# Performance work log

Measured on AMD Instinct MI355X. Metric: run time of the kernel, lower is better.

Reference implementation:

```python
import jax, jax.numpy as jnp
import numpy as np

N_NODES = 100000
N_EDGES = 1600000
D_IN = 128
D_OUT = 128


def setup_inputs() -> dict:
    key = jax.random.key(0)
    k1, k2, k3, k4, k5, k6 = jax.random.split(key, 6)
    x = jax.random.normal(k1, (N_NODES, D_IN), dtype=jnp.float32)
    edge_src = jax.random.randint(k2, (N_EDGES,), 0, N_NODES, dtype=jnp.int64 if jax.config.jax_enable_x64 else jnp.int32)
    edge_dst = jax.random.randint(k3, (N_EDGES,), 0, N_NODES, dtype=jnp.int64 if jax.config.jax_enable_x64 else jnp.int32)
    edge_val = jax.random.uniform(k4, (N_EDGES,), dtype=jnp.float32)
    # nn.Linear(2*D_IN, D_OUT): store W as [2*D_IN, D_OUT] (transposed torch layout)
    W = jax.random.normal(k5, (2 * D_IN, D_OUT), dtype=jnp.float32) * (1.0 / np.sqrt(2 * D_IN))
    b = jax.random.normal(k6, (D_OUT,), dtype=jnp.float32) * 0.01
    return {"x": x, "edge_src": edge_src, "edge_dst": edge_dst, "edge_val": edge_val, "W": W, "b": b}


def reference(x, edge_src, edge_dst, edge_val, W, b):
    # support = adj @ x  (sparse COO: adj[dst, src] = edge_val)
    gathered = x[edge_src] * edge_val[:, None]               # [E, D_IN]
    support = jax.ops.segment_sum(gathered, edge_dst, num_segments=x.shape[0])  # [N, D_IN]
    # concat self + aggregated neighbor features, then linear
    h = jnp.concatenate([x, support], axis=1)                # [N, 2*D_IN]
    return h @ W + b                                          # [N, D_OUT]
```

## Files before the change

### kernel.cpp

```cpp
#include <hip/hip_runtime.h>

#define D 128
#define NBMAX 2048
#define CHUNK 2048
#define BN 64
#define GCAP 2048

typedef __attribute__((ext_vector_type(8))) short bf16x8;
typedef __attribute__((ext_vector_type(4))) float f32x4;

__device__ __forceinline__ unsigned short f2bf(float f) {
    unsigned int u = __builtin_bit_cast(unsigned int, f);
    u = (u + 0x7fffu + ((u >> 16) & 1u)) >> 16;
    return (unsigned short)u;
}
__device__ __forceinline__ float bf2f(unsigned int u) {
    return __builtin_bit_cast(float, u << 16);
}

__global__ void zero_int_kernel(int* __restrict__ p, int n) {
    int i = blockIdx.x * 256 + threadIdx.x;
    if (i < n) p[i] = 0;
}

__global__ void xprep_kernel(const float* __restrict__ x,
                             unsigned short* __restrict__ x_bf, int n4) {
    int i = blockIdx.x * 256 + threadIdx.x;
    if (i >= n4) return;
    float4 v = ((const float4*)x)[i];
    ushort4 s; s.x = f2bf(v.x); s.y = f2bf(v.y); s.z = f2bf(v.z); s.w = f2bf(v.w);
    ((ushort4*)x_bf)[i] = s;
}

__global__ void wprep_kernel(const float* __restrict__ W,
                             unsigned short* __restrict__ WT) {
    int t = blockIdx.x * 256 + threadIdx.x;
    int col = t & 127, k = t >> 7;
    WT[col * 256 + k] = f2bf(W[k * D + col]);
}

__global__ __launch_bounds__(256) void bhist_kernel(const int* __restrict__ edst,
                                                    int* __restrict__ bucket_cnt,
                                                    int E, int NB) {
    __shared__ int h[NBMAX];
    for (int i = threadIdx.x; i < NB; i += 256) h[i] = 0;
    __syncthreads();
    int stride = gridDim.x * 256;
    for (int e = blockIdx.x * 256 + threadIdx.x; e < E; e += stride)
        atomicAdd(&h[edst[e] >> 6], 1);
    __syncthreads();
    for (int i = threadIdx.x; i < NB; i += 256) {
        int c = h[i];
        if (c) atomicAdd(&bucket_cnt[i], c);
    }
}

__global__ __launch_bounds__(256) void bscan_kernel(const int* __restrict__ cnt,
                                                    int* __restrict__ base,
                                                    int* __restrict__ cursor, int NB) {
    __shared__ int p[256];
    int t = threadIdx.x;
    int c[8]; int loc = 0;
#pragma unroll
    for (int k = 0; k < 8; ++k) {
        int i = t * 8 + k;
        c[k] = (i < NB) ? cnt[i] : 0;
        loc += c[k];
    }
    p[t] = loc;
    __syncthreads();
    for (int off = 1; off < 256; off <<= 1) {
        int v = p[t];
        int u = (t >= off) ? p[t - off] : 0;
        __syncthreads();
        p[t] = v + u;
        __syncthreads();
    }
    int ex = p[t] - loc;
#pragma unroll
    for (int k = 0; k < 8; ++k) {
        int i = t * 8 + k;
        if (i < NB) { base[i] = ex; cursor[i] = ex; }
        ex += c[k];
    }
}

__global__ __launch_bounds__(256) void bfill_kernel(const int* __restrict__ esrc,
                                                    const int* __restrict__ edst,
                                                    const float* __restrict__ eval,
                                                    int* __restrict__ bucket_cursor,
                                                    int2* __restrict__ edge_pack,
                                                    int E, int NB) {
    __shared__ int lh[NBMAX];
    __shared__ int lcur[NBMAX];
    __shared__ int p[256];
    __shared__ int2 ord[CHUNK];
    __shared__ unsigned short obk[CHUNK];

    const int tid = threadIdx.x;
    const int base = blockIdx.x * CHUNK;
    const int n = min(CHUNK, E - base);

    for (int i = tid; i < NBMAX; i += 256) lh[i] = 0;
    __syncthreads();

    int esv[8]; int ebk[8];
    float evv[8];
#pragma unroll
    for (int k = 0; k < 8; ++k) {
        int li = k * 256 + tid;
        if (li < n) {
            int i = base + li;
            int dst = edst[i];
            esv[k] = esrc[i];
            evv[k] = eval[i];
            int b = dst >> 6;
            ebk[k] = b | ((dst & 63) << 16);
            atomicAdd(&lh[b], 1);
        } else ebk[k] = -1;
    }
    __syncthreads();

    int s[8]; int loc = 0;
#pragma unroll
    for (int k = 0; k < 8; ++k) { s[k] = lh[8 * tid + k]; loc += s[k]; }
    p[tid] = loc;
    __syncthreads();
    for (int off = 1; off < 256; off <<= 1) {
        int v = p[tid];
        int u = (tid >= off) ? p[tid - off] : 0;
        __syncthreads();
        p[tid] = v + u;
        __syncthreads();
    }
    int ex = p[tid] - loc;
#pragma unroll
    for (int k = 0; k < 8; ++k) { lcur[8 * tid + k] = ex; ex += s[k]; }
    __syncthreads();

#pragma unroll
    for (int k = 0; k < 8; ++k) {
        if (ebk[k] >= 0) {
            int b = ebk[k] & 0xffff, nl = ebk[k] >> 16;
            int slot = atomicAdd(&lcur[b], 1);
            ord[slot] = make_int2(esv[k] | (nl << 20), __builtin_bit_cast(int, evv[k]));
            obk[slot] = (unsigned short)b;
        }
    }
    __syncthreads();

    for (int b = tid; b < NB; b += 256) {
        int c = lh[b];
        if (c) lh[b] = atomicAdd(&bucket_cursor[b], c) - (lcur[b] - c);
    }
    __syncthreads();

    for (int i = tid; i < n; i += 256) {
        int b = obk[i];
        edge_pack[lh[b] + i] = ord[i];
    }
}

__global__ __launch_bounds__(256, 4) void gather_fused_kernel(
        const unsigned short* __restrict__ x_bf,
        const int* __restrict__ bucket_base,
        const int* __restrict__ bucket_cnt,
        const int2* __restrict__ edge_pack,
        const unsigned short* __restrict__ WT,
        const float* __restrict__ bias,
        float* __restrict__ out, int N) {
    __shared__ unsigned short accb[BN * 136];
    __shared__ int2 ord[GCAP];
    __shared__ int cnt64[BN];
    __shared__ int start64[BN + 1];
    __shared__ int cur64[BN];

    const int tid = threadIdx.x;
    const int b = blockIdx.x;
    const int start = bucket_base[b];
    const int cnt = bucket_cnt[b];
    const int node0 = b * BN;
    const int w = tid >> 6, lane = tid & 63;
    unsigned int* accw = (unsigned int*)accb;

    for (int i = tid * 8; i < BN * 136; i += 2048)
        *(uint4*)(accb + i) = make_uint4(0u, 0u, 0u, 0u);

    for (int c0 = 0; c0 < cnt; c0 += GCAP) {
        const int n = min(GCAP, cnt - c0);
        if (tid < BN) cnt64[tid] = 0;
        __syncthreads();
        for (int i = tid; i < n; i += 256)
            atomicAdd(&cnt64[(edge_pack[start + c0 + i].x >> 20) & 63], 1);
        __syncthreads();
        if (tid < BN) {
            int c = cnt64[tid];
            int v = c;
#pragma unroll
            for (int off = 1; off < 64; off <<= 1) {
                int t = __shfl_up(v, off, 64);
                if (lane >= off) v += t;
            }
            start64[tid] = v - c;
            cur64[tid] = v - c;
            if (tid == BN - 1) start64[BN] = v;
        }
        __syncthreads();
        for (int i = tid; i < n; i += 256) {
            int2 e = edge_pack[start + c0 + i];
            ord[atomicAdd(&cur64[(e.x >> 20) & 63], 1)] = e;
        }
        __syncthreads();

        const int js = start64[w * 16];
        const int je = start64[w * 16 + 16];
        int cur = -1;
        float ax = 0.f, ay = 0.f;
        for (int g = js; g < je; g += 16) {
            int m = je - g; if (m > 16) m = 16;
            int2 e[16];
#pragma unroll
            for (int k = 0; k < 16; ++k) {
                int idx = g + k; if (idx >= je) idx = je - 1;
                e[k] = ord[idx];
            }
            unsigned int p[16];
#pragma unroll
            for (int k = 0; k < 16; ++k)
                p[k] = *(const unsigned int*)(x_bf + (size_t)(e[k].x & 0xFFFFF) * D + lane * 2);
#pragma unroll
            for (int k = 0; k < 16; ++k) {
                if (k < m) {
                    int nd = (e[k].x >> 20) & 63;
                    if (nd != cur) {
                        if (cur >= 0) {
                            unsigned int o = accw[cur * 68 + lane];
                            float o0 = bf2f(o & 0xffffu) + ax;
                            float o1 = bf2f(o >> 16) + ay;
                            accw[cur * 68 + lane] =
                                (unsigned int)f2bf(o0) | ((unsigned int)f2bf(o1) << 16);
                        }
                        cur = nd; ax = 0.f; ay = 0.f;
                    }
                    float v = __builtin_bit_cast(float, e[k].y);
                    ax += bf2f(p[k] & 0xffffu) * v;
                    ay += bf2f(p[k] >> 16) * v;
                }
            }
        }
        if (cur >= 0) {
            unsigned int o = accw[cur * 68 + lane];
            float o0 = bf2f(o & 0xffffu) + ax;
            float o1 = bf2f(o >> 16) + ay;
            accw[cur * 68 + lane] = (unsigned int)f2bf(o0) | ((unsigned int)f2bf(o1) << 16);
        }
        __syncthreads();
    }

    const int quad = lane >> 4;
    const int l15  = lane & 15;
    const int colbase = w * 32;

    f32x4 acc[4][2];
#pragma unroll
    for (int rt = 0; rt < 4; ++rt) {
        acc[rt][0] = (f32x4){0.f, 0.f, 0.f, 0.f};
        acc[rt][1] = (f32x4){0.f, 0.f, 0.f, 0.f};
    }

#pragma unroll
    for (int ks = 0; ks < 8; ++ks) {
        bf16x8 wf0 = *(const bf16x8*)(WT + (size_t)(colbase + l15) * 256 + ks * 32 + quad * 8);
        bf16x8 wf1 = *(const bf16x8*)(WT + (size_t)(colbase + 16 + l15) * 256 + ks * 32 + quad * 8);
#pragma unroll
        for (int rt = 0; rt < 4; ++rt) {
            int row = rt * 16 + l15;
            bf16x8 a;
            if (ks < 4) {
                int rg = node0 + row; if (rg >= N) rg = N - 1;
                a = *(const bf16x8*)(x_bf + (size_t)rg * D + ks * 32 + quad * 8);
            } else {
                a = *(const bf16x8*)(accb + row * 136 + (ks - 4) * 32 + quad * 8);
            }
            acc[rt][0] = __builtin_amdgcn_mfma_f32_16x16x32_bf16(a, wf0, acc[rt][0], 0, 0, 0);
            acc[rt][1] = __builtin_amdgcn_mfma_f32_16x16x32_bf16(a, wf1, acc[rt][1], 0, 0, 0);
        }
    }

#pragma unroll
    for (int ct = 0; ct < 2; ++ct) {
        int col = colbase + ct * 16 + l15;
        float bv = bias[col];
#pragma unroll
        for (int rt = 0; rt < 4; ++rt) {
#pragma unroll
            for (int rg = 0; rg < 4; ++rg) {
                int row = node0 + rt * 16 + quad * 4 + rg;
                if (row < N)
                    out[(size_t)row * D + col] = acc[rt][ct][rg] + bv;
            }
        }
    }
}

extern "C" void kernel_launch(void* const* d_in, const int* in_sizes, int n_in,
                              void* d_out, int out_size, void* d_ws, size_t ws_size,
                              hipStream_t stream) {
    const float* x    = (const float*)d_in[0];
    const int*   esrc = (const int*)d_in[1];
    const int*   edst = (const int*)d_in[2];
    const float* eval = (const float*)d_in[3];
    const float* W    = (const float*)d_in[4];
    const float* bias = (const float*)d_in[5];
    float*       out  = (float*)d_out;

    const int N = in_sizes[0] / D;
    const int E = in_sizes[1];
    const int NB = (N + BN - 1) / BN;

    char* ws = (char*)d_ws;
    unsigned short* x_bf       = (unsigned short*)ws;
    int2*           edge_pack  = (int2*)(ws + 25600000);
    unsigned short* WT         = (unsigned short*)(ws + 38400000);
    int*            bucket_cnt = (int*)(ws + 38465536);
    int*            bucket_base= (int*)(ws + 38473728);
    int*            bucket_cur = (int*)(ws + 38481920);

    zero_int_kernel<<<(NB + 255) / 256, 256, 0, stream>>>(bucket_cnt, NB);
    xprep_kernel<<<(N * D / 4 + 255) / 256, 256, 0, stream>>>(x, x_bf, N * D / 4);
    wprep_kernel<<<(2 * D * D) / 256, 256, 0, stream>>>(W, WT);
    bhist_kernel<<<512, 256, 0, stream>>>(edst, bucket_cnt, E, NB);
    bscan_kernel<<<1, 256, 0, stream>>>(bucket_cnt, bucket_base, bucket_cur, NB);
    bfill_kernel<<<(E + CHUNK - 1) / CHUNK, 256, 0, stream>>>(esrc, edst, eval,
                                                              bucket_cur, edge_pack, E, NB);
    gather_fused_kernel<<<NB, 256, 0, stream>>>(x_bf, bucket_base, bucket_cnt,
                                                edge_pack, WT, bias, out, N);
}
```

Before: 274.8 us.

## Replace bucket sort with per-node counting sort and simplify gather

```diff
diff --git a/kernel.cpp b/kernel.cpp
--- a/kernel.cpp
+++ b/kernel.cpp
@@ -1,10 +1,7 @@
 #include <hip/hip_runtime.h>
 
 #define D 128
-#define NBMAX 2048
-#define CHUNK 2048
 #define BN 64
-#define GCAP 2048
 
 typedef __attribute__((ext_vector_type(8))) short bf16x8;
 typedef __attribute__((ext_vector_type(4))) float f32x4;
@@ -18,55 +15,93 @@
     return __builtin_bit_cast(float, u << 16);
 }
 
-__global__ void zero_int_kernel(int* __restrict__ p, int n) {
-    int i = blockIdx.x * 256 + threadIdx.x;
-    if (i < n) p[i] = 0;
-}
-
-__global__ void xprep_kernel(const float* __restrict__ x,
-                             unsigned short* __restrict__ x_bf, int n4) {
-    int i = blockIdx.x * 256 + threadIdx.x;
-    if (i >= n4) return;
-    float4 v = ((const float4*)x)[i];
-    ushort4 s; s.x = f2bf(v.x); s.y = f2bf(v.y); s.z = f2bf(v.z); s.w = f2bf(v.w);
-    ((ushort4*)x_bf)[i] = s;
-}
-
-__global__ void wprep_kernel(const float* __restrict__ W,
-                             unsigned short* __restrict__ WT) {
-    int t = blockIdx.x * 256 + threadIdx.x;
-    int col = t & 127, k = t >> 7;
-    WT[col * 256 + k] = f2bf(W[k * D + col]);
-}
-
-__global__ __launch_bounds__(256) void bhist_kernel(const int* __restrict__ edst,
-                                                    int* __restrict__ bucket_cnt,
-                                                    int E, int NB) {
-    __shared__ int h[NBMAX];
-    for (int i = threadIdx.x; i < NB; i += 256) h[i] = 0;
-    __syncthreads();
+__global__ void prep_kernel(const float* __restrict__ x,
+                            unsigned short* __restrict__ x_bf,
+                            const float* __restrict__ W,
+                            unsigned short* __restrict__ WT,
+                            int* __restrict__ nc,
+                            int n4, int XB, int WB, int NN) {
+    int blk = blockIdx.x, tid = threadIdx.x;
+    if (blk < XB) {
+        int i = blk * 256 + tid;
+        if (i < n4) {
+            float4 v = ((const float4*)x)[i];
+            ushort4 s;
+            s.x = f2bf(v.x); s.y = f2bf(v.y); s.z = f2bf(v.z); s.w = f2bf(v.w);
+            ((ushort4*)x_bf)[i] = s;
+        }
+    } else if (blk < XB + WB) {
+        int t = (blk - XB) * 256 + tid;
+        if (t < 2 * D * D) {
+            int col = t & 127, k = t >> 7;
+            WT[col * 256 + k] = f2bf(W[k * D + col]);
+        }
+    } else {
+        int i = (blk - XB - WB) * 256 + tid;
+        if (i < NN) nc[i] = 0;
+    }
+}
+
+__global__ void nhist_kernel(const int* __restrict__ edst,
+                             int* __restrict__ nc, int E) {
     int stride = gridDim.x * 256;
-    for (int e = blockIdx.x * 256 + threadIdx.x; e < E; e += stride)
-        atomicAdd(&h[edst[e] >> 6], 1);
-    __syncthreads();
-    for (int i = threadIdx.x; i < NB; i += 256) {
-        int c = h[i];
-        if (c) atomicAdd(&bucket_cnt[i], c);
-    }
-}
-
-__global__ __launch_bounds__(256) void bscan_kernel(const int* __restrict__ cnt,
-                                                    int* __restrict__ base,
-                                                    int* __restrict__ cursor, int NB) {
+    for (int i = blockIdx.x * 256 + threadIdx.x; i < E; i += stride)
+        atomicAdd(&nc[edst[i]], 1);
+}
+
+__global__ __launch_bounds__(256) void scanA_kernel(const int* __restrict__ nc,
+                                                    int* __restrict__ psum, int NN) {
     __shared__ int p[256];
     int t = threadIdx.x;
-    int c[8]; int loc = 0;
-#pragma unroll
-    for (int k = 0; k < 8; ++k) {
-        int i = t * 8 + k;
-        c[k] = (i < NB) ? cnt[i] : 0;
-        loc += c[k];
-    }
+    int i0 = blockIdx.x * 1024 + t * 4;
+    int s = 0;
+    if (i0 + 3 < NN) {
+        int4 v = *(const int4*)(nc + i0);
+        s = v.x + v.y + v.z + v.w;
+    } else {
+#pragma unroll
+        for (int k = 0; k < 4; ++k) { int i = i0 + k; if (i < NN) s += nc[i]; }
+    }
+    p[t] = s;
+    __syncthreads();
+    for (int off = 128; off > 0; off >>= 1) {
+        if (t < off) p[t] += p[t + off];
+        __syncthreads();
+    }
+    if (t == 0) psum[blockIdx.x] = p[0];
+}
+
+__global__ void scanB_kernel(const int* __restrict__ psum,
+                             int* __restrict__ pbase, int nparts) {
+    __shared__ int q[128];
+    int t = threadIdx.x;
+    int s = (t < nparts) ? psum[t] : 0;
+    q[t] = s;
+    __syncthreads();
+    for (int off = 1; off < 128; off <<= 1) {
+        int v = q[t];
+        int u = (t >= off) ? q[t - off] : 0;
+        __syncthreads();
+        q[t] = v + u;
+        __syncthreads();
+    }
+    if (t < nparts) pbase[t] = q[t] - s;
+}
+
+__global__ __launch_bounds__(256) void scanC_kernel(int* __restrict__ nc,
+                                                    const int* __restrict__ pbase, int NN) {
+    __shared__ int p[256];
+    int t = threadIdx.x, blk = blockIdx.x;
+    int i0 = blk * 1024 + t * 4;
+    int c[4];
+    if (i0 + 3 < NN) {
+        int4 v = *(const int4*)(nc + i0);
+        c[0] = v.x; c[1] = v.y; c[2] = v.z; c[3] = v.w;
+    } else {
+#pragma unroll
+        for (int k = 0; k < 4; ++k) { int i = i0 + k; c[k] = (i < NN) ? nc[i] : 0; }
+    }
+    int loc = c[0] + c[1] + c[2] + c[3];
     p[t] = loc;
     __syncthreads();
     for (int off = 1; off < 256; off <<= 1) {
@@ -76,186 +111,88 @@
         p[t] = v + u;
         __syncthreads();
     }
-    int ex = p[t] - loc;
-#pragma unroll
-    for (int k = 0; k < 8; ++k) {
-        int i = t * 8 + k;
-        if (i < NB) { base[i] = ex; cursor[i] = ex; }
-        ex += c[k];
-    }
-}
-
-__global__ __launch_bounds__(256) void bfill_kernel(const int* __restrict__ esrc,
-                                                    const int* __restrict__ edst,
-                                                    const float* __restrict__ eval,
-                                                    int* __restrict__ bucket_cursor,
-                                                    int2* __restrict__ edge_pack,
-                                                    int E, int NB) {
-    __shared__ int lh[NBMAX];
-    __shared__ int lcur[NBMAX];
-    __shared__ int p[256];
-    __shared__ int2 ord[CHUNK];
-    __shared__ unsigned short obk[CHUNK];
-
-    const int tid = threadIdx.x;
-    const int base = blockIdx.x * CHUNK;
-    const int n = min(CHUNK, E - base);
-
-    for (int i = tid; i < NBMAX; i += 256) lh[i] = 0;
-    __syncthreads();
-
-    int esv[8]; int ebk[8];
-    float evv[8];
-#pragma unroll
-    for (int k = 0; k < 8; ++k) {
-        int li = k * 256 + tid;
-        if (li < n) {
-            int i = base + li;
-            int dst = edst[i];
-            esv[k] = esrc[i];
-            evv[k] = eval[i];
-            int b = dst >> 6;
-            ebk[k] = b | ((dst & 63) << 16);
-            atomicAdd(&lh[b], 1);
-        } else ebk[k] = -1;
-    }
-    __syncthreads();
-
-    int s[8]; int loc = 0;
-#pragma unroll
-    for (int k = 0; k < 8; ++k) { s[k] = lh[8 * tid + k]; loc += s[k]; }
-    p[tid] = loc;
-    __syncthreads();
-    for (int off = 1; off < 256; off <<= 1) {
-        int v = p[tid];
-        int u = (tid >= off) ? p[tid - off] : 0;
-        __syncthreads();
-        p[tid] = v + u;
-        __syncthreads();
-    }
-    int ex = p[tid] - loc;
-#pragma unroll
-    for (int k = 0; k < 8; ++k) { lcur[8 * tid + k] = ex; ex += s[k]; }
-    __syncthreads();
-
-#pragma unroll
-    for (int k = 0; k < 8; ++k) {
-        if (ebk[k] >= 0) {
-            int b = ebk[k] & 0xffff, nl = ebk[k] >> 16;
-            int slot = atomicAdd(&lcur[b], 1);
-            ord[slot] = make_int2(esv[k] | (nl << 20), __builtin_bit_cast(int, evv[k]));
-            obk[slot] = (unsigned short)b;
-        }
-    }
-    __syncthreads();
-
-    for (int b = tid; b < NB; b += 256) {
-        int c = lh[b];
-        if (c) lh[b] = atomicAdd(&bucket_cursor[b], c) - (lcur[b] - c);
-    }
-    __syncthreads();
-
-    for (int i = tid; i < n; i += 256) {
-        int b = obk[i];
-        edge_pack[lh[b] + i] = ord[i];
-    }
-}
-
-__global__ __launch_bounds__(256, 4) void gather_fused_kernel(
+    int ex = p[t] - loc + pbase[blk];
+    int4 o;
+    ex += c[0]; o.x = ex;
+    ex += c[1]; o.y = ex;
+    ex += c[2]; o.z = ex;
+    ex += c[3]; o.w = ex;
+    *(int4*)(nc + i0) = o;
+}
+
+__global__ void nscatter_kernel(const int* __restrict__ esrc,
+                                const int* __restrict__ edst,
+                                const float* __restrict__ eval,
+                                int* __restrict__ nc,
+                                int2* __restrict__ edge_pack, int E) {
+    int stride = gridDim.x * 256;
+    for (int i = blockIdx.x * 256 + threadIdx.x; i < E; i += stride) {
+        int dst = edst[i];
+        int src = esrc[i];
+        float v = eval[i];
+        int pos = atomicSub(&nc[dst], 1) - 1;
+        edge_pack[pos] = make_int2((src << 8) | (dst & 63), __builtin_bit_cast(int, v));
+    }
+}
+
+__global__ __launch_bounds__(256, 8) void gather_fused_kernel(
         const unsigned short* __restrict__ x_bf,
-        const int* __restrict__ bucket_base,
-        const int* __restrict__ bucket_cnt,
+        const int* __restrict__ node_start,
         const int2* __restrict__ edge_pack,
         const unsigned short* __restrict__ WT,
         const float* __restrict__ bias,
         float* __restrict__ out, int N) {
     __shared__ unsigned short accb[BN * 136];
-    __shared__ int2 ord[GCAP];
-    __shared__ int cnt64[BN];
-    __shared__ int start64[BN + 1];
-    __shared__ int cur64[BN];
+    __shared__ int nb[BN + 1];
 
     const int tid = threadIdx.x;
     const int b = blockIdx.x;
-    const int start = bucket_base[b];
-    const int cnt = bucket_cnt[b];
     const int node0 = b * BN;
     const int w = tid >> 6, lane = tid & 63;
     unsigned int* accw = (unsigned int*)accb;
 
     for (int i = tid * 8; i < BN * 136; i += 2048)
         *(uint4*)(accb + i) = make_uint4(0u, 0u, 0u, 0u);
-
-    for (int c0 = 0; c0 < cnt; c0 += GCAP) {
-        const int n = min(GCAP, cnt - c0);
-        if (tid < BN) cnt64[tid] = 0;
-        __syncthreads();
-        for (int i = tid; i < n; i += 256)
-            atomicAdd(&cnt64[(edge_pack[start + c0 + i].x >> 20) & 63], 1);
-        __syncthreads();
-        if (tid < BN) {
-            int c = cnt64[tid];
-            int v = c;
-#pragma unroll
-            for (int off = 1; off < 64; off <<= 1) {
-                int t = __shfl_up(v, off, 64);
-                if (lane >= off) v += t;
+    if (tid <= BN) nb[tid] = node_start[node0 + tid];
+    __syncthreads();
+
+    const int js = __builtin_amdgcn_readfirstlane(nb[w * 16]);
+    const int je = __builtin_amdgcn_readfirstlane(nb[w * 16 + 16]);
+    const unsigned short* xl = x_bf + lane * 2;
+
+    int cur = -1;
+    float ax = 0.f, ay = 0.f;
+    for (int g = js; g < je; g += 16) {
+        int m = je - g; if (m > 16) m = 16;
+        int2 e[16];
+#pragma unroll
+        for (int k = 0; k < 16; ++k) {
+            int idx = g + k; if (idx >= je) idx = je - 1;
+            e[k] = edge_pack[idx];
+        }
+        unsigned int p[16];
+#pragma unroll
+        for (int k = 0; k < 16; ++k)
+            p[k] = *(const unsigned int*)(xl + ((e[k].x >> 8) << 7));
+#pragma unroll
+        for (int k = 0; k < 16; ++k) {
+            if (k < m) {
+                int nd = e[k].x & 63;
+                if (nd != cur) {
+                    if (cur >= 0)
+                        accw[cur * 68 + lane] =
+                            (unsigned int)f2bf(ax) | ((unsigned int)f2bf(ay) << 16);
+                    cur = nd; ax = 0.f; ay = 0.f;
+                }
+                float v = __builtin_bit_cast(float, e[k].y);
+                ax += bf2f(p[k] & 0xffffu) * v;
+                ay += bf2f(p[k] >> 16) * v;
             }
-            start64[tid] = v - c;
-            cur64[tid] = v - c;
-            if (tid == BN - 1) start64[BN] = v;
-        }
-        __syncthreads();
-        for (int i = tid; i < n; i += 256) {
-            int2 e = edge_pack[start + c0 + i];
-            ord[atomicAdd(&cur64[(e.x >> 20) & 63], 1)] = e;
-        }
-        __syncthreads();
-
-        const int js = start64[w * 16];
-        const int je = start64[w * 16 + 16];
-        int cur = -1;
-        float ax = 0.f, ay = 0.f;
-        for (int g = js; g < je; g += 16) {
-            int m = je - g; if (m > 16) m = 16;
-            int2 e[16];
-#pragma unroll
-            for (int k = 0; k < 16; ++k) {
-                int idx = g + k; if (idx >= je) idx = je - 1;
-                e[k] = ord[idx];
-            }
-            unsigned int p[16];
-#pragma unroll
-            for (int k = 0; k < 16; ++k)
-                p[k] = *(const unsigned int*)(x_bf + (size_t)(e[k].x & 0xFFFFF) * D + lane * 2);
-#pragma unroll
-            for (int k = 0; k < 16; ++k) {
-                if (k < m) {
-                    int nd = (e[k].x >> 20) & 63;
-                    if (nd != cur) {
-                        if (cur >= 0) {
-                            unsigned int o = accw[cur * 68 + lane];
-                            float o0 = bf2f(o & 0xffffu) + ax;
-                            float o1 = bf2f(o >> 16) + ay;
-                            accw[cur * 68 + lane] =
-                                (unsigned int)f2bf(o0) | ((unsigned int)f2bf(o1) << 16);
-                        }
-                        cur = nd; ax = 0.f; ay = 0.f;
-                    }
-                    float v = __builtin_bit_cast(float, e[k].y);
-                    ax += bf2f(p[k] & 0xffffu) * v;
-                    ay += bf2f(p[k] >> 16) * v;
-                }
-            }
-        }
-        if (cur >= 0) {
-            unsigned int o = accw[cur * 68 + lane];
-            float o0 = bf2f(o & 0xffffu) + ax;
-            float o1 = bf2f(o >> 16) + ay;
-            accw[cur * 68 + lane] = (unsigned int)f2bf(o0) | ((unsigned int)f2bf(o1) << 16);
-        }
-        __syncthreads();
-    }
+        }
+    }
+    if (cur >= 0)
+        accw[cur * 68 + lane] = (unsigned int)f2bf(ax) | ((unsigned int)f2bf(ay) << 16);
+    __syncthreads();
 
     const int quad = lane >> 4;
     const int l15  = lane & 15;
@@ -314,25 +251,30 @@
     const float* bias = (const float*)d_in[5];
     float*       out  = (float*)d_out;
 
-    const int N = in_sizes[0] / D;
-    const int E = in_sizes[1];
+    const int N  = in_sizes[0] / D;
+    const int E  = in_sizes[1];
     const int NB = (N + BN - 1) / BN;
+    const int NSB = (N + 1023) / 1024;
 
     char* ws = (char*)d_ws;
-    unsigned short* x_bf       = (unsigned short*)ws;
-    int2*           edge_pack  = (int2*)(ws + 25600000);
-    unsigned short* WT         = (unsigned short*)(ws + 38400000);
-    int*            bucket_cnt = (int*)(ws + 38465536);
-    int*            bucket_base= (int*)(ws + 38473728);
-    int*            bucket_cur = (int*)(ws + 38481920);
-
-    zero_int_kernel<<<(NB + 255) / 256, 256, 0, stream>>>(bucket_cnt, NB);
-    xprep_kernel<<<(N * D / 4 + 255) / 256, 256, 0, stream>>>(x, x_bf, N * D / 4);
-    wprep_kernel<<<(2 * D * D) / 256, 256, 0, stream>>>(W, WT);
-    bhist_kernel<<<512, 256, 0, stream>>>(edst, bucket_cnt, E, NB);
-    bscan_kernel<<<1, 256, 0, stream>>>(bucket_cnt, bucket_base, bucket_cur, NB);
-    bfill_kernel<<<(E + CHUNK - 1) / CHUNK, 256, 0, stream>>>(esrc, edst, eval,
-                                                              bucket_cur, edge_pack, E, NB);
-    gather_fused_kernel<<<NB, 256, 0, stream>>>(x_bf, bucket_base, bucket_cnt,
-                                                edge_pack, WT, bias, out, N);
-}
+    unsigned short* x_bf      = (unsigned short*)ws;
+    int2*           edge_pack = (int2*)(ws + 25600000);
+    unsigned short* WT        = (unsigned short*)(ws + 38400000);
+    int*            nc        = (int*)(ws + 38465536);
+    int*            psum      = (int*)(ws + 38866944);
+    int*            pbase     = (int*)(ws + 38867456);
+
+    const int n4 = N * D / 4;
+    const int XB = (n4 + 255) / 256;
+    const int WB = (2 * D * D + 255) / 256;
+    const int ZB = (N + 255) / 256;
+
+    prep_kernel<<<XB + WB + ZB, 256, 0, stream>>>(x, x_bf, W, WT, nc, n4, XB, WB, N);
+    nhist_kernel<<<1024, 256, 0, stream>>>(edst, nc, E);
+    scanA_kernel<<<NSB, 256, 0, stream>>>(nc, psum, N);
+    scanB_kernel<<<1, 128, 0, stream>>>(psum, pbase, NSB);
+    scanC_kernel<<<NSB, 256, 0, stream>>>(nc, pbase, N);
+    nscatter_kernel<<<1024, 256, 0, stream>>>(esrc, edst, eval, nc, edge_pack, E);
+    gather_fused_kernel<<<NB, 256, 0, stream>>>(x_bf, nc, edge_pack, WT, bias, out, N);
+    (void)ws_size; (void)n_in; (void)out_size;
+}
```

Result: slower. 383.9 us (+39.7%).
